# Kernel optimization log

Measured on AMD Instinct MI355X. Metric: run time of the kernel, lower is better.

Reference implementation:

```python
import jax, jax.numpy as jnp
import numpy as np

TOP_K = 2


def setup_inputs() -> dict:
    key = jax.random.key(0)
    kx, ke, kg, kn = jax.random.split(key, 4)
    B, T, D, E = 4, 4096, 2048, 64
    scale = 1.0 / np.sqrt(D)
    return {
        "x": jax.random.normal(kx, (B, T, D), dtype=jnp.float32),
        "eps": jax.random.normal(ke, (B, T, E), dtype=jnp.float32),
        "Wg_w": jax.random.normal(kg, (E, D), dtype=jnp.float32) * scale,
        "Wg_b": jnp.zeros((E,), dtype=jnp.float32),
        "Wn_w": jax.random.normal(kn, (E, D), dtype=jnp.float32) * scale,
        "Wn_b": jnp.zeros((E,), dtype=jnp.float32),
    }


def reference(x, eps, Wg_w, Wg_b, Wn_w, Wn_b):
    # gate/noise logits: [B, T, E]
    gate = jnp.einsum("btd,ed->bte", x, Wg_w) + Wg_b
    noise = jnp.einsum("btd,ed->bte", x, Wn_w) + Wn_b
    h = gate + eps * jax.nn.softplus(noise)

    topk_vals, topk_idxs = jax.lax.top_k(h, TOP_K)  # [B, T, k]
    B, T, E = h.shape
    g = jnp.full_like(h, -jnp.inf)
    g = g.at[jnp.arange(B)[:, None, None],
             jnp.arange(T)[None, :, None],
             topk_idxs].set(topk_vals)
    return jax.nn.softmax(g, axis=-1)
```

## Files before the change

### kernel.cpp

```cpp
#include <hip/hip_runtime.h>
#include <math.h>

typedef float fx4    __attribute__((ext_vector_type(4)));
typedef float f32x16 __attribute__((ext_vector_type(16)));
typedef short bf16x8 __attribute__((ext_vector_type(8)));
typedef unsigned int ux4 __attribute__((ext_vector_type(4)));

#define TM    64
#define DDIM  2048
#define ENUM  64

__device__ __forceinline__ unsigned short bf16_rne(float f) {
    unsigned int u = __builtin_bit_cast(unsigned int, f);
    unsigned int r = u + 0x7FFFu + ((u >> 16) & 1u);
    return (unsigned short)(r >> 16);
}
__device__ __forceinline__ float bf16_f32(unsigned short h) {
    unsigned int u = ((unsigned int)h) << 16;
    return __builtin_bit_cast(float, u);
}

__global__ __launch_bounds__(256)
void convert_w(const float* __restrict__ Wg, const float* __restrict__ Wn,
               unsigned short* __restrict__ wsB) {
    const int t  = blockIdx.x * 256 + threadIdx.x;
    const int l  = t & 63;
    const int ct = (t >> 6) & 3;
    const int kt = t >> 8;
    const int col = ct * 32 + (l & 31);
    const int k0  = kt * 16 + (l >> 5) * 8;
    const float* src = ((col < ENUM) ? (Wg + (size_t)col * DDIM)
                                     : (Wn + (size_t)(col - ENUM) * DDIM)) + k0;
    bf16x8 vh, vm;
    #pragma unroll
    for (int j = 0; j < 8; ++j) {
        float v = src[j];
        unsigned short h = bf16_rne(v);
        float r1 = v - bf16_f32(h);
        unsigned short m = bf16_rne(r1);
        vh[j] = (short)h; vm[j] = (short)m;
    }
    *(bf16x8*)(wsB + ((size_t)(0 * 32768 + t)) * 8) = vh;
    *(bf16x8*)(wsB + ((size_t)(1 * 32768 + t)) * 8) = vm;
}

__device__ __forceinline__ void split2x8_cvt(fx4 a, fx4 b, bf16x8& H, bf16x8& M) {
    const float e0[4] = {a[0], a[2], b[0], b[2]};
    const float e1[4] = {a[1], a[3], b[1], b[3]};
    ux4 hw, mw;
    #pragma unroll
    for (int j = 0; j < 4; ++j) {
        float v0 = e0[j], v1 = e1[j];
        unsigned h;
        asm("v_cvt_pk_bf16_f32 %0, %1, %2" : "=v"(h) : "v"(v0), "v"(v1));
        float h0 = __builtin_bit_cast(float, h << 16);
        float h1 = __builtin_bit_cast(float, h & 0xFFFF0000u);
        float r0 = v0 - h0, r1 = v1 - h1;
        unsigned m;
        asm("v_cvt_pk_bf16_f32 %0, %1, %2" : "=v"(m) : "v"(r0), "v"(r1));
        hw[j] = h; mw[j] = m;
    }
    H = __builtin_bit_cast(bf16x8, hw);
    M = __builtin_bit_cast(bf16x8, mw);
}

#define MFMA32 __builtin_amdgcn_mfma_f32_32x32x16_bf16

__global__ __launch_bounds__(512, 2)
void noisy_topk_mfma(const float* __restrict__ x,
                     const float* __restrict__ eps,
                     const float* __restrict__ gb,
                     const float* __restrict__ nb,
                     const unsigned short* __restrict__ wsB,
                     float* __restrict__ out)
{
    __shared__ float hbuf[TM][132];
    __shared__ float pv1[TM][8], pv2[TM][8];
    __shared__ int   pi1[TM][8], pi2[TM][8];
    __shared__ float tp1[TM], tp2[TM];
    __shared__ int   ti1[TM], ti2[TM];

    const int tid  = threadIdx.x;
    const int lane = tid & 63;
    const int wv   = tid >> 6;
    const int rt   = wv & 1;
    const int kh   = wv >> 1;
    const int bs   = (blockIdx.x & 7) * 32 + (blockIdx.x >> 3);
    const int row0 = bs * TM;

    const int r32 = lane & 31;
    const int k8  = (lane >> 5) * 8;

    const float* xa = x + (size_t)(row0 + rt * 32 + r32) * DDIM + kh * 512 + k8;

    const unsigned short* bq = wsB + ((size_t)(kh * 32) * 4) * 512 + lane * 8;

    f32x16 ac0 = {}, ac1 = {}, ac2 = {}, ac3 = {};

    fx4 A0_0, A0_1, A1_0, A1_1;
    bf16x8 B0[8], B1[8];

    #define LDA(n, kt) do { \
        n##_0 = *(const fx4*)(xa + (kt) * 16); \
        n##_1 = *(const fx4*)(xa + (kt) * 16 + 4); \
    } while (0)

    #define LDB(B, kt) do { \
        const unsigned short* _p = bq + (size_t)(kt) * 2048; \
        B[0] = *(const bf16x8*)(_p);                  \
        B[1] = *(const bf16x8*)(_p + 262144);         \
        B[2] = *(const bf16x8*)(_p + 512);            \
        B[3] = *(const bf16x8*)(_p + 512 + 262144);   \
        B[4] = *(const bf16x8*)(_p + 1024);           \
        B[5] = *(const bf16x8*)(_p + 1024 + 262144);  \
        B[6] = *(const bf16x8*)(_p + 1536);           \
        B[7] = *(const bf16x8*)(_p + 1536 + 262144);  \
    } while (0)

    #define KTILE(n, B) do { \
        bf16x8 Ah, Am; \
        split2x8_cvt(n##_0, n##_1, Ah, Am); \
        __builtin_amdgcn_s_setprio(1); \
        ac0 = MFMA32(Ah, B[0], ac0, 0, 0, 0); ac1 = MFMA32(Ah, B[2], ac1, 0, 0, 0); \
        ac2 = MFMA32(Ah, B[4], ac2, 0, 0, 0); ac3 = MFMA32(Ah, B[6], ac3, 0, 0, 0); \
        ac0 = MFMA32(Ah, B[1], ac0, 0, 0, 0); ac1 = MFMA32(Ah, B[3], ac1, 0, 0, 0); \
        ac2 = MFMA32(Ah, B[5], ac2, 0, 0, 0); ac3 = MFMA32(Ah, B[7], ac3, 0, 0, 0); \
        ac0 = MFMA32(Am, B[0], ac0, 0, 0, 0); ac1 = MFMA32(Am, B[2], ac1, 0, 0, 0); \
        ac2 = MFMA32(Am, B[4], ac2, 0, 0, 0); ac3 = MFMA32(Am, B[6], ac3, 0, 0, 0); \
        ac0 = MFMA32(Am, B[1], ac0, 0, 0, 0); ac1 = MFMA32(Am, B[3], ac1, 0, 0, 0); \
        ac2 = MFMA32(Am, B[5], ac2, 0, 0, 0); ac3 = MFMA32(Am, B[7], ac3, 0, 0, 0); \
        __builtin_amdgcn_s_setprio(0); \
    } while (0)

    LDA(A0, 0); LDB(B0, 0);
    LDA(A1, 1); LDB(B1, 1);

    for (int kt = 0; kt < 32; kt += 2) {
        const bool more = (kt + 2 < 32);
        KTILE(A0, B0);
        if (more) { LDA(A0, kt + 2); LDB(B0, kt + 2); }
        KTILE(A1, B1);
        if (more) { LDA(A1, kt + 3); LDB(B1, kt + 3); }
    }

    #undef KTILE
    #undef LDB
    #undef LDA

    const int rowb = rt * 32 + 4 * (lane >> 5);
    if (kh == 0) {
        #pragma unroll
        for (int r = 0; r < 16; ++r) {
            const int row = (r & 3) + 8 * (r >> 2) + rowb;
            hbuf[row][r32]      = ac0[r];
            hbuf[row][r32 + 32] = ac1[r];
            hbuf[row][r32 + 64] = ac2[r];
            hbuf[row][r32 + 96] = ac3[r];
        }
    }
    __syncthreads();
    #pragma unroll
    for (int ph = 1; ph < 4; ++ph) {
        if (kh == ph) {
            #pragma unroll
            for (int r = 0; r < 16; ++r) {
                const int row = (r & 3) + 8 * (r >> 2) + rowb;
                hbuf[row][r32]      += ac0[r];
                hbuf[row][r32 + 32] += ac1[r];
                hbuf[row][r32 + 64] += ac2[r];
                hbuf[row][r32 + 96] += ac3[r];
            }
        }
        __syncthreads();
    }

    const int rloc = tid >> 3;
    const int q    = tid & 7;
    {
        float v1 = -INFINITY, v2 = -INFINITY;
        int   i1 = -1, i2 = -1;
        const float* ep = eps + (size_t)(row0 + rloc) * ENUM + q * 8;
        #pragma unroll
        for (int v = 0; v < 2; ++v) {
            fx4 gv  = *(const fx4*)&hbuf[rloc][q * 8 + v * 4];
            fx4 nv  = *(const fx4*)&hbuf[rloc][ENUM + q * 8 + v * 4];
            fx4 ev  = *(const fx4*)(ep + v * 4);
            fx4 gbv = *(const fx4*)(gb + q * 8 + v * 4);
            fx4 nbv = *(const fx4*)(nb + q * 8 + v * 4);
            #pragma unroll
            for (int j = 0; j < 4; ++j) {
                float nz = nv[j] + nbv[j];
                float sp = fmaxf(nz, 0.f) + log1pf(expf(-fabsf(nz)));
                float h  = gv[j] + gbv[j] + ev[j] * sp;
                int   e  = q * 8 + v * 4 + j;
                if (h > v1)      { v2 = v1; i2 = i1; v1 = h; i1 = e; }
                else if (h > v2) { v2 = h;  i2 = e; }
            }
        }
        pv1[rloc][q] = v1; pv2[rloc][q] = v2;
        pi1[rloc][q] = i1; pi2[rloc][q] = i2;
    }
    __syncthreads();

    if (tid < TM) {
        float v1 = -INFINITY, v2 = -INFINITY;
        int   i1 = -1, i2 = -1;
        #pragma unroll
        for (int qq = 0; qq < 8; ++qq) {
            float a1 = pv1[tid][qq]; int b1 = pi1[tid][qq];
            float a2 = pv2[tid][qq]; int b2 = pi2[tid][qq];
            if (a1 > v1)      { v2 = v1; i2 = i1; v1 = a1; i1 = b1; }
            else if (a1 > v2) { v2 = a1; i2 = b1; }
            if (a2 > v1)      { v2 = v1; i2 = i1; v1 = a2; i1 = b2; }
            else if (a2 > v2) { v2 = a2; i2 = b2; }
        }
        float e2  = expf(v2 - v1);
        float inv = 1.f / (1.f + e2);
        tp1[tid] = inv;
        tp2[tid] = e2 * inv;
        ti1[tid] = i1; ti2[tid] = i2;
    }
    __syncthreads();

    {
        const int   orow = tid >> 3;
        const int   oq   = tid & 7;
        const int   a1 = ti1[orow], a2 = ti2[orow];
        const float p1 = tp1[orow], p2 = tp2[orow];
        float* op = out + (size_t)(row0 + orow) * ENUM + oq * 8;
        #pragma unroll
        for (int v = 0; v < 2; ++v) {
            fx4 o;
            #pragma unroll
            for (int j = 0; j < 4; ++j) {
                int e = oq * 8 + v * 4 + j;
                o[j] = (e == a1) ? p1 : ((e == a2) ? p2 : 0.f);
            }
            *(fx4*)(op + v * 4) = o;
        }
    }
}

extern "C" void kernel_launch(void* const* d_in, const int* in_sizes, int n_in,
                              void* d_out, int out_size, void* d_ws, size_t ws_size,
                              hipStream_t stream) {
    const float* x   = (const float*)d_in[0];
    const float* eps = (const float*)d_in[1];
    const float* Wg  = (const float*)d_in[2];
    const float* gbp = (const float*)d_in[3];
    const float* Wn  = (const float*)d_in[4];
    const float* nbp = (const float*)d_in[5];
    float* out = (float*)d_out;
    unsigned short* wsB = (unsigned short*)d_ws;

    hipLaunchKernelGGL(convert_w, dim3(128), dim3(256), 0, stream, Wg, Wn, wsB);

    const int M = in_sizes[0] / DDIM;
    hipLaunchKernelGGL(noisy_topk_mfma, dim3(M / TM), dim3(512), 0, stream,
                       x, eps, gbp, nbp, wsB, out);
}
```

Baseline: 57.50 us.

## Halve row tile to 32 and split K across eight waves

Reduces the rows per block from 64 to 32, giving twice as many blocks, and assigns each of the eight waves a 256-wide K slice instead of splitting waves between two row tiles and four K quarters. The A prefetch is deepened to four register sets while B stays double-buffered, and the epilogue is remapped to 16 threads per row. This targets better CU occupancy and load balance across the grid. The cost is that each B weight fetch is reused by half as many rows, and the cross-wave reduction through LDS takes eight serialized phases.

```diff
diff --git a/kernel.cpp b/kernel.cpp
--- a/kernel.cpp
+++ b/kernel.cpp
@@ -6,7 +6,7 @@
 typedef short bf16x8 __attribute__((ext_vector_type(8)));
 typedef unsigned int ux4 __attribute__((ext_vector_type(4)));
 
-#define TM    64
+#define TM    32
 #define DDIM  2048
 #define ENUM  64
 
@@ -75,29 +75,27 @@
                      float* __restrict__ out)
 {
     __shared__ float hbuf[TM][132];
-    __shared__ float pv1[TM][8], pv2[TM][8];
-    __shared__ int   pi1[TM][8], pi2[TM][8];
+    __shared__ float pv1[TM][16], pv2[TM][16];
+    __shared__ int   pi1[TM][16], pi2[TM][16];
     __shared__ float tp1[TM], tp2[TM];
     __shared__ int   ti1[TM], ti2[TM];
 
     const int tid  = threadIdx.x;
     const int lane = tid & 63;
-    const int wv   = tid >> 6;
-    const int rt   = wv & 1;
-    const int kh   = wv >> 1;
-    const int bs   = (blockIdx.x & 7) * 32 + (blockIdx.x >> 3);
+    const int kh   = tid >> 6;
+    const int bs   = (blockIdx.x & 7) * 64 + (blockIdx.x >> 3);
     const int row0 = bs * TM;
 
     const int r32 = lane & 31;
     const int k8  = (lane >> 5) * 8;
 
-    const float* xa = x + (size_t)(row0 + rt * 32 + r32) * DDIM + kh * 512 + k8;
-
-    const unsigned short* bq = wsB + ((size_t)(kh * 32) * 4) * 512 + lane * 8;
+    const float* xa = x + (size_t)(row0 + r32) * DDIM + kh * 256 + k8;
+
+    const unsigned short* bq = wsB + ((size_t)(kh * 16) * 4) * 512 + lane * 8;
 
     f32x16 ac0 = {}, ac1 = {}, ac2 = {}, ac3 = {};
 
-    fx4 A0_0, A0_1, A1_0, A1_1;
+    fx4 A0_0, A0_1, A1_0, A1_1, A2_0, A2_1, A3_0, A3_1;
     bf16x8 B0[8], B1[8];
 
     #define LDA(n, kt) do { \
@@ -132,22 +130,29 @@
         __builtin_amdgcn_s_setprio(0); \
     } while (0)
 
-    LDA(A0, 0); LDB(B0, 0);
-    LDA(A1, 1); LDB(B1, 1);
-
-    for (int kt = 0; kt < 32; kt += 2) {
-        const bool more = (kt + 2 < 32);
+    LDA(A0, 0); LDA(A1, 1); LDA(A2, 2); LDA(A3, 3);
+    LDB(B0, 0); LDB(B1, 1);
+
+    for (int kt = 0; kt < 16; kt += 4) {
         KTILE(A0, B0);
-        if (more) { LDA(A0, kt + 2); LDB(B0, kt + 2); }
+        if (kt + 4 < 16) LDA(A0, kt + 4);
+        if (kt + 2 < 16) LDB(B0, kt + 2);
         KTILE(A1, B1);
-        if (more) { LDA(A1, kt + 3); LDB(B1, kt + 3); }
+        if (kt + 5 < 16) LDA(A1, kt + 5);
+        if (kt + 3 < 16) LDB(B1, kt + 3);
+        KTILE(A2, B0);
+        if (kt + 6 < 16) LDA(A2, kt + 6);
+        if (kt + 4 < 16) LDB(B0, kt + 4);
+        KTILE(A3, B1);
+        if (kt + 7 < 16) LDA(A3, kt + 7);
+        if (kt + 5 < 16) LDB(B1, kt + 5);
     }
 
     #undef KTILE
     #undef LDB
     #undef LDA
 
-    const int rowb = rt * 32 + 4 * (lane >> 5);
+    const int rowb = 4 * (lane >> 5);
     if (kh == 0) {
         #pragma unroll
         for (int r = 0; r < 16; ++r) {
@@ -160,7 +165,7 @@
     }
     __syncthreads();
     #pragma unroll
-    for (int ph = 1; ph < 4; ++ph) {
+    for (int ph = 1; ph < 8; ++ph) {
         if (kh == ph) {
             #pragma unroll
             for (int r = 0; r < 16; ++r) {
@@ -174,28 +179,25 @@
         __syncthreads();
     }
 
-    const int rloc = tid >> 3;
-    const int q    = tid & 7;
+    const int rloc = tid >> 4;
+    const int q    = tid & 15;
     {
         float v1 = -INFINITY, v2 = -INFINITY;
         int   i1 = -1, i2 = -1;
-        const float* ep = eps + (size_t)(row0 + rloc) * ENUM + q * 8;
-        #pragma unroll
-        for (int v = 0; v < 2; ++v) {
-            fx4 gv  = *(const fx4*)&hbuf[rloc][q * 8 + v * 4];
-            fx4 nv  = *(const fx4*)&hbuf[rloc][ENUM + q * 8 + v * 4];
-            fx4 ev  = *(const fx4*)(ep + v * 4);
-            fx4 gbv = *(const fx4*)(gb + q * 8 + v * 4);
-            fx4 nbv = *(const fx4*)(nb + q * 8 + v * 4);
-            #pragma unroll
-            for (int j = 0; j < 4; ++j) {
-                float nz = nv[j] + nbv[j];
-                float sp = fmaxf(nz, 0.f) + log1pf(expf(-fabsf(nz)));
-                float h  = gv[j] + gbv[j] + ev[j] * sp;
-                int   e  = q * 8 + v * 4 + j;
-                if (h > v1)      { v2 = v1; i2 = i1; v1 = h; i1 = e; }
-                else if (h > v2) { v2 = h;  i2 = e; }
-            }
+        const float* ep = eps + (size_t)(row0 + rloc) * ENUM + q * 4;
+        fx4 gv  = *(const fx4*)&hbuf[rloc][q * 4];
+        fx4 nv  = *(const fx4*)&hbuf[rloc][ENUM + q * 4];
+        fx4 ev  = *(const fx4*)(ep);
+        fx4 gbv = *(const fx4*)(gb + q * 4);
+        fx4 nbv = *(const fx4*)(nb + q * 4);
+        #pragma unroll
+        for (int j = 0; j < 4; ++j) {
+            float nz = nv[j] + nbv[j];
+            float sp = fmaxf(nz, 0.f) + log1pf(expf(-fabsf(nz)));
+            float h  = gv[j] + gbv[j] + ev[j] * sp;
+            int   e  = q * 4 + j;
+            if (h > v1)      { v2 = v1; i2 = i1; v1 = h; i1 = e; }
+            else if (h > v2) { v2 = h;  i2 = e; }
         }
         pv1[rloc][q] = v1; pv2[rloc][q] = v2;
         pi1[rloc][q] = i1; pi2[rloc][q] = i2;
@@ -206,7 +208,7 @@
         float v1 = -INFINITY, v2 = -INFINITY;
         int   i1 = -1, i2 = -1;
         #pragma unroll
-        for (int qq = 0; qq < 8; ++qq) {
+        for (int qq = 0; qq < 16; ++qq) {
             float a1 = pv1[tid][qq]; int b1 = pi1[tid][qq];
             float a2 = pv2[tid][qq]; int b2 = pi2[tid][qq];
             if (a1 > v1)      { v2 = v1; i2 = i1; v1 = a1; i1 = b1; }
@@ -223,21 +225,18 @@
     __syncthreads();
 
     {
-        const int   orow = tid >> 3;
-        const int   oq   = tid & 7;
+        const int   orow = tid >> 4;
+        const int   oq   = tid & 15;
         const int   a1 = ti1[orow], a2 = ti2[orow];
         const float p1 = tp1[orow], p2 = tp2[orow];
-        float* op = out + (size_t)(row0 + orow) * ENUM + oq * 8;
-        #pragma unroll
-        for (int v = 0; v < 2; ++v) {
-            fx4 o;
-            #pragma unroll
-            for (int j = 0; j < 4; ++j) {
-                int e = oq * 8 + v * 4 + j;
-                o[j] = (e == a1) ? p1 : ((e == a2) ? p2 : 0.f);
-            }
-            *(fx4*)(op + v * 4) = o;
-        }
+        float* op = out + (size_t)(row0 + orow) * ENUM + oq * 4;
+        fx4 o;
+        #pragma unroll
+        for (int j = 0; j < 4; ++j) {
+            int e = oq * 4 + j;
+            o[j] = (e == a1) ? p1 : ((e == a2) ? p2 : 0.f);
+        }
+        *(fx4*)(op) = o;
     }
 }
 
```

Result: slower. 68.83 us (+19.7%).

## Split waves across column tiles instead of four-way K split

Applied to the files above, without the earlier changes.

Work is now split as 2 row tiles x 2 column halves x 2 K halves instead of 2 row tiles x 4 K quarters. Each wave holds two accumulators instead of four and walks twice as many K steps with half the B loads per step. This cuts the LDS reduction from four serialized phases to two and lowers register pressure. In exchange, each wave now loads and converts its A row slice for twice as many K steps, so the same x data is read by both column-half waves, and the longer K loop reduces overlap per wave.

```diff
diff --git a/kernel.cpp b/kernel.cpp
--- a/kernel.cpp
+++ b/kernel.cpp
@@ -84,21 +84,23 @@
     const int lane = tid & 63;
     const int wv   = tid >> 6;
     const int rt   = wv & 1;
-    const int kh   = wv >> 1;
+    const int ct2  = (wv >> 1) & 1;
+    const int kh   = wv >> 2;
     const int bs   = (blockIdx.x & 7) * 32 + (blockIdx.x >> 3);
     const int row0 = bs * TM;
 
     const int r32 = lane & 31;
     const int k8  = (lane >> 5) * 8;
-
-    const float* xa = x + (size_t)(row0 + rt * 32 + r32) * DDIM + kh * 512 + k8;
-
-    const unsigned short* bq = wsB + ((size_t)(kh * 32) * 4) * 512 + lane * 8;
-
-    f32x16 ac0 = {}, ac1 = {}, ac2 = {}, ac3 = {};
+    const int ctA = ct2 * 2;
+
+    const float* xa = x + (size_t)(row0 + rt * 32 + r32) * DDIM + kh * 1024 + k8;
+
+    const unsigned short* bq = wsB + (((size_t)(kh * 64) * 4) + ctA) * 512 + lane * 8;
+
+    f32x16 ac0 = {}, ac1 = {};
 
     fx4 A0_0, A0_1, A1_0, A1_1;
-    bf16x8 B0[8], B1[8];
+    bf16x8 B0[4], B1[4];
 
     #define LDA(n, kt) do { \
         n##_0 = *(const fx4*)(xa + (kt) * 16); \
@@ -108,35 +110,27 @@
     #define LDB(B, kt) do { \
         const unsigned short* _p = bq + (size_t)(kt) * 2048; \
         B[0] = *(const bf16x8*)(_p);                  \
-        B[1] = *(const bf16x8*)(_p + 262144);         \
-        B[2] = *(const bf16x8*)(_p + 512);            \
+        B[1] = *(const bf16x8*)(_p + 512);            \
+        B[2] = *(const bf16x8*)(_p + 262144);         \
         B[3] = *(const bf16x8*)(_p + 512 + 262144);   \
-        B[4] = *(const bf16x8*)(_p + 1024);           \
-        B[5] = *(const bf16x8*)(_p + 1024 + 262144);  \
-        B[6] = *(const bf16x8*)(_p + 1536);           \
-        B[7] = *(const bf16x8*)(_p + 1536 + 262144);  \
     } while (0)
 
     #define KTILE(n, B) do { \
         bf16x8 Ah, Am; \
         split2x8_cvt(n##_0, n##_1, Ah, Am); \
         __builtin_amdgcn_s_setprio(1); \
-        ac0 = MFMA32(Ah, B[0], ac0, 0, 0, 0); ac1 = MFMA32(Ah, B[2], ac1, 0, 0, 0); \
-        ac2 = MFMA32(Ah, B[4], ac2, 0, 0, 0); ac3 = MFMA32(Ah, B[6], ac3, 0, 0, 0); \
-        ac0 = MFMA32(Ah, B[1], ac0, 0, 0, 0); ac1 = MFMA32(Ah, B[3], ac1, 0, 0, 0); \
-        ac2 = MFMA32(Ah, B[5], ac2, 0, 0, 0); ac3 = MFMA32(Ah, B[7], ac3, 0, 0, 0); \
-        ac0 = MFMA32(Am, B[0], ac0, 0, 0, 0); ac1 = MFMA32(Am, B[2], ac1, 0, 0, 0); \
-        ac2 = MFMA32(Am, B[4], ac2, 0, 0, 0); ac3 = MFMA32(Am, B[6], ac3, 0, 0, 0); \
-        ac0 = MFMA32(Am, B[1], ac0, 0, 0, 0); ac1 = MFMA32(Am, B[3], ac1, 0, 0, 0); \
-        ac2 = MFMA32(Am, B[5], ac2, 0, 0, 0); ac3 = MFMA32(Am, B[7], ac3, 0, 0, 0); \
+        ac0 = MFMA32(Ah, B[0], ac0, 0, 0, 0); ac1 = MFMA32(Ah, B[1], ac1, 0, 0, 0); \
+        ac0 = MFMA32(Ah, B[2], ac0, 0, 0, 0); ac1 = MFMA32(Ah, B[3], ac1, 0, 0, 0); \
+        ac0 = MFMA32(Am, B[0], ac0, 0, 0, 0); ac1 = MFMA32(Am, B[1], ac1, 0, 0, 0); \
+        ac0 = MFMA32(Am, B[2], ac0, 0, 0, 0); ac1 = MFMA32(Am, B[3], ac1, 0, 0, 0); \
         __builtin_amdgcn_s_setprio(0); \
     } while (0)
 
     LDA(A0, 0); LDB(B0, 0);
     LDA(A1, 1); LDB(B1, 1);
 
-    for (int kt = 0; kt < 32; kt += 2) {
-        const bool more = (kt + 2 < 32);
+    for (int kt = 0; kt < 64; kt += 2) {
+        const bool more = (kt + 2 < 64);
         KTILE(A0, B0);
         if (more) { LDA(A0, kt + 2); LDB(B0, kt + 2); }
         KTILE(A1, B1);
@@ -148,31 +142,25 @@
     #undef LDA
 
     const int rowb = rt * 32 + 4 * (lane >> 5);
+    const int colA = ctA * 32 + r32;
     if (kh == 0) {
         #pragma unroll
         for (int r = 0; r < 16; ++r) {
             const int row = (r & 3) + 8 * (r >> 2) + rowb;
-            hbuf[row][r32]      = ac0[r];
-            hbuf[row][r32 + 32] = ac1[r];
-            hbuf[row][r32 + 64] = ac2[r];
-            hbuf[row][r32 + 96] = ac3[r];
-        }
-    }
-    __syncthreads();
-    #pragma unroll
-    for (int ph = 1; ph < 4; ++ph) {
-        if (kh == ph) {
-            #pragma unroll
-            for (int r = 0; r < 16; ++r) {
-                const int row = (r & 3) + 8 * (r >> 2) + rowb;
-                hbuf[row][r32]      += ac0[r];
-                hbuf[row][r32 + 32] += ac1[r];
-                hbuf[row][r32 + 64] += ac2[r];
-                hbuf[row][r32 + 96] += ac3[r];
-            }
-        }
-        __syncthreads();
-    }
+            hbuf[row][colA]      = ac0[r];
+            hbuf[row][colA + 32] = ac1[r];
+        }
+    }
+    __syncthreads();
+    if (kh == 1) {
+        #pragma unroll
+        for (int r = 0; r < 16; ++r) {
+            const int row = (r & 3) + 8 * (r >> 2) + rowb;
+            hbuf[row][colA]      += ac0[r];
+            hbuf[row][colA + 32] += ac1[r];
+        }
+    }
+    __syncthreads();
 
     const int rloc = tid >> 3;
     const int q    = tid & 7;
```

After: 64.95 us. 1.13x slower.
